# Kernel tuning notes

Hardware: AMD Instinct MI355X
Metric: run time of the kernel (lower is better)

The kernel has to match this reference:

```python
import jax, jax.numpy as jnp
import numpy as np

B, T, NPTS_PER, C, XDIM, YDIM, HEADS = 2, 4, 32768, 128, 200, 200, 4


def setup_inputs() -> dict:
    key = jax.random.key(0)
    ks = jax.random.split(key, 6)
    npts = B * T * NPTS_PER
    features = jax.random.normal(ks[0], (npts, C), dtype=jnp.float32)
    # chunk j of size NPTS_PER holds points of combined (batch*T + time) index j
    col0 = jnp.repeat(jnp.arange(B * T, dtype=jnp.int32), NPTS_PER)
    colx = jax.random.randint(ks[1], (npts,), 0, XDIM, dtype=jnp.int32)
    coly = jax.random.randint(ks[2], (npts,), 0, YDIM, dtype=jnp.int32)
    indices = jnp.stack([col0, colx, coly], axis=1)  # (Npts, 3)
    temp_embed = jax.random.normal(ks[3], (T, C), dtype=jnp.float32) * 0.02
    w_qkv = jax.random.normal(ks[4], (C, 3 * C), dtype=jnp.float32) / np.sqrt(C).astype(np.float32)
    w_out = jax.random.normal(ks[5], (C, C), dtype=jnp.float32) / np.sqrt(C).astype(np.float32)
    return {"features": features, "indices": indices, "temp_embed": temp_embed,
            "w_qkv": w_qkv, "w_out": w_out, "b": B, "t": T}


def reference(features, indices, temp_embed, w_qkv, w_out, b, t):
    npts, c = features.shape
    n = npts // (b * t)
    hd = c // HEADS
    scale = 1.0 / float(np.sqrt(hd))

    # temporal embedding: features + temp_embed[indices[:,0] % t]
    time_idx = indices[:, 0] % t
    f = features + temp_embed[time_idx]

    # chunk(b*t) + stack + rearrange 'N (b t) c -> (b N) t c'
    f = f.reshape(b, t, n, c).transpose(0, 2, 1, 3).reshape(b * n, t, c)

    # layer: multi-head self-attention over the temporal axis, take position t-1
    qkv = f @ w_qkv  # (bN, t, 3c)
    q, k, v = jnp.split(qkv, 3, axis=-1)
    split = lambda x: x.reshape(b * n, t, HEADS, hd).transpose(0, 2, 1, 3)  # (bN, H, t, hd)
    q, k, v = split(q), split(k), split(v)
    attn = jax.nn.softmax(jnp.einsum('bhqd,bhkd->bhqk', q, k) * scale, axis=-1)
    o = jnp.einsum('bhqk,bhkd->bhqd', attn, v)
    o = o.transpose(0, 2, 1, 3).reshape(b * n, t, c) @ w_out
    feat_out = o[:, t - 1]  # (bN, c)

    # indices: indices[:,0] //= t ; same window rearrange ; keep slice t-1
    idx = indices.at[:, 0].set(indices[:, 0] // t)
    idx_out = idx.reshape(b, t, n, 3).transpose(0, 2, 1, 3).reshape(b * n, t, 3)[:, t - 1]
    return feat_out, idx_out
```

## Files before the change

### kernel.cpp

```cpp
#include <hip/hip_runtime.h>

#define NPER   32768
#define TT     4
#define CDIM   128
#define NSEQ   65536
#define FEAT_OUT_ELEMS (NSEQ * CDIM)

constexpr int TSEQ = 16;
constexpr int ROWS = TSEQ * TT;
constexpr int KV_STRIDE = 257;
constexpr int Q_STRIDE  = 129;
constexpr int O_STRIDE  = 132;

typedef __attribute__((ext_vector_type(8))) short  short8;
typedef __attribute__((ext_vector_type(4))) float  f32x4;

__device__ __forceinline__ unsigned short f2bf(float x) {
    unsigned u = __float_as_uint(x);
    u = (u + 0x7FFFu + ((u >> 16) & 1u)) >> 16;
    return (unsigned short)u;
}
__device__ __forceinline__ float bf2f(unsigned short h) {
    return __uint_as_float(((unsigned)h) << 16);
}


__global__ void tqkv_kernel(const float* __restrict__ temp_embed,
                            const float* __restrict__ w_qkv,
                            float* __restrict__ tqkv) {
    int tid = blockIdx.x * blockDim.x + threadIdx.x;
    if (tid >= TT * 384) return;
    int t = tid / 384, col = tid - t * 384;
    float acc = 0.f;
#pragma unroll 8
    for (int k = 0; k < CDIM; ++k)
        acc = fmaf(temp_embed[t * CDIM + k], w_qkv[k * 384 + col], acc);
    tqkv[t * 384 + col] = acc;
}

__global__ void prep_weights(const float* __restrict__ w_qkv,
                             const float* __restrict__ w_out,
                             unsigned short* __restrict__ wkT_hi,
                             unsigned short* __restrict__ wkT_lo,
                             unsigned short* __restrict__ woT_hi,
                             unsigned short* __restrict__ woT_lo) {
    int id = blockIdx.x * 256 + threadIdx.x;
    if (id < 384 * 128) {
        int col = id >> 7, k = id & 127;
        float x = w_qkv[k * 384 + col];
        unsigned short h = f2bf(x);
        wkT_hi[id] = h;
        wkT_lo[id] = f2bf(x - bf2f(h));
    } else {
        int j = id - 384 * 128;
        int col = j >> 7, k = j & 127;
        float x = w_out[k * CDIM + col];
        unsigned short h = f2bf(x);
        woT_hi[j] = h;
        woT_lo[j] = f2bf(x - bf2f(h));
    }
}

__global__ __launch_bounds__(512, 2) void fused_mfma(
    const float* __restrict__ feat,
    const int*   __restrict__ indices,
    const float* __restrict__ tqkv,
    const unsigned short* __restrict__ wkT_hi,
    const unsigned short* __restrict__ wkT_lo,
    const unsigned short* __restrict__ woT_hi,
    const unsigned short* __restrict__ woT_lo,
    float* __restrict__ out) {

    __shared__ unsigned short AsH[ROWS * CDIM];
    __shared__ unsigned short AsL[ROWS * CDIM];
    __shared__ float KVs[ROWS * KV_STRIDE];
    __shared__ float Qs[TSEQ * Q_STRIDE];
    __shared__ float Os[TSEQ * O_STRIDE];
    __shared__ int   tix[ROWS];

    const int tid  = threadIdx.x;
    const int seq0 = blockIdx.x * TSEQ;

#pragma unroll
    for (int i = 0; i < 4; ++i) {
        int idx = tid + i * 512;
        int row = idx >> 5, c4 = idx & 31;
        int s = seq0 + (row >> 2), t = row & 3;
        int b = s >> 15, n = s & (NPER - 1);
        size_t p = (size_t)(b * TT + t) * NPER + n;
        float4 v = *reinterpret_cast<const float4*>(feat + p * CDIM + c4 * 4);
        unsigned short h0 = f2bf(v.x), h1 = f2bf(v.y), h2 = f2bf(v.z), h3 = f2bf(v.w);
        unsigned short l0 = f2bf(v.x - bf2f(h0)), l1 = f2bf(v.y - bf2f(h1));
        unsigned short l2 = f2bf(v.z - bf2f(h2)), l3 = f2bf(v.w - bf2f(h3));
        unsigned off = (unsigned)(row * 256 + c4 * 8) ^ ((unsigned)(row & 7) << 4);
        uint2 hp; hp.x = (unsigned)h0 | ((unsigned)h1 << 16); hp.y = (unsigned)h2 | ((unsigned)h3 << 16);
        uint2 lp; lp.x = (unsigned)l0 | ((unsigned)l1 << 16); lp.y = (unsigned)l2 | ((unsigned)l3 << 16);
        *reinterpret_cast<uint2*>(reinterpret_cast<char*>(AsH) + off) = hp;
        *reinterpret_cast<uint2*>(reinterpret_cast<char*>(AsL) + off) = lp;
        if (c4 == 0) tix[row] = indices[p * 3] & (TT - 1);
    }
    __syncthreads();

    const int w  = tid >> 6, l = tid & 63;
    const int lr = l & 15,  lh = l >> 4;

    f32x4 accKV[4][2];
#pragma unroll
    for (int mt = 0; mt < 4; ++mt)
#pragma unroll
        for (int j = 0; j < 2; ++j) accKV[mt][j] = (f32x4){0.f, 0.f, 0.f, 0.f};

#pragma unroll
    for (int kt = 0; kt < 4; ++kt) {
        const int kb = kt * 32 + lh * 8;
        const int c0 = (128 + (2 * w) * 16 + lr) * 128 + kb;
        const int c1 = c0 + 16 * 128;
        short8 B0h = *reinterpret_cast<const short8*>(wkT_hi + c0);
        short8 B0l = *reinterpret_cast<const short8*>(wkT_lo + c0);
        short8 B1h = *reinterpret_cast<const short8*>(wkT_hi + c1);
        short8 B1l = *reinterpret_cast<const short8*>(wkT_lo + c1);
#pragma unroll
        for (int mt = 0; mt < 4; ++mt) {
            int row = mt * 16 + lr;
            unsigned off = (unsigned)(row * 256 + kt * 64 + lh * 16) ^ ((unsigned)(row & 7) << 4);
            short8 Ah = *reinterpret_cast<const short8*>(reinterpret_cast<const char*>(AsH) + off);
            short8 Al = *reinterpret_cast<const short8*>(reinterpret_cast<const char*>(AsL) + off);
            accKV[mt][0] = __builtin_amdgcn_mfma_f32_16x16x32_bf16(Ah, B0h, accKV[mt][0], 0, 0, 0);
            accKV[mt][0] = __builtin_amdgcn_mfma_f32_16x16x32_bf16(Al, B0h, accKV[mt][0], 0, 0, 0);
            accKV[mt][0] = __builtin_amdgcn_mfma_f32_16x16x32_bf16(Ah, B0l, accKV[mt][0], 0, 0, 0);
            accKV[mt][1] = __builtin_amdgcn_mfma_f32_16x16x32_bf16(Ah, B1h, accKV[mt][1], 0, 0, 0);
            accKV[mt][1] = __builtin_amdgcn_mfma_f32_16x16x32_bf16(Al, B1h, accKV[mt][1], 0, 0, 0);
            accKV[mt][1] = __builtin_amdgcn_mfma_f32_16x16x32_bf16(Ah, B1l, accKV[mt][1], 0, 0, 0);
        }
    }
#pragma unroll
    for (int mt = 0; mt < 4; ++mt)
#pragma unroll
        for (int j = 0; j < 2; ++j) {
            int col = (2 * w + j) * 16 + lr;
#pragma unroll
            for (int r = 0; r < 4; ++r) {
                int row = mt * 16 + lh * 4 + r;
                int te  = tix[row];
                KVs[row * KV_STRIDE + col] = accKV[mt][j][r] + tqkv[te * 384 + 128 + col];
            }
        }

    f32x4 accQ = (f32x4){0.f, 0.f, 0.f, 0.f};
#pragma unroll
    for (int kt = 0; kt < 4; ++kt) {
        const int kb = kt * 32 + lh * 8;
        const int cq = (w * 16 + lr) * 128 + kb;
        short8 Bh = *reinterpret_cast<const short8*>(wkT_hi + cq);
        short8 Bl = *reinterpret_cast<const short8*>(wkT_lo + cq);
        int row = 4 * lr + 3;
        unsigned off = (unsigned)(row * 256 + kt * 64 + lh * 16) ^ ((unsigned)(row & 7) << 4);
        short8 Ah = *reinterpret_cast<const short8*>(reinterpret_cast<const char*>(AsH) + off);
        short8 Al = *reinterpret_cast<const short8*>(reinterpret_cast<const char*>(AsL) + off);
        accQ = __builtin_amdgcn_mfma_f32_16x16x32_bf16(Ah, Bh, accQ, 0, 0, 0);
        accQ = __builtin_amdgcn_mfma_f32_16x16x32_bf16(Al, Bh, accQ, 0, 0, 0);
        accQ = __builtin_amdgcn_mfma_f32_16x16x32_bf16(Ah, Bl, accQ, 0, 0, 0);
    }
#pragma unroll
    for (int r = 0; r < 4; ++r) {
        int s = lh * 4 + r, col = w * 16 + lr;
        int te = tix[4 * s + 3];
        Qs[s * Q_STRIDE + col] = accQ[r] + tqkv[te * 384 + col];
    }
    __syncthreads();

    {
        const float scale = 0.17677669529663687f;
        int pr = tid >> 3, j = tid & 7;
        int ls = pr >> 2, h = pr & 3;
        int d0 = h * 32 + j * 4;
        const float* qp = &Qs[ls * Q_STRIDE + d0];
        float q0 = qp[0], q1 = qp[1], q2 = qp[2], q3 = qp[3];
        float sc[4];
#pragma unroll
        for (int t2 = 0; t2 < 4; ++t2) {
            const float* kr = &KVs[(ls * 4 + t2) * KV_STRIDE + d0];
            float sum = fmaf(q0, kr[0], fmaf(q1, kr[1], fmaf(q2, kr[2], q3 * kr[3])));
            sum += __shfl_xor(sum, 1);
            sum += __shfl_xor(sum, 2);
            sum += __shfl_xor(sum, 4);
            sc[t2] = sum * scale;
        }
        float m = fmaxf(fmaxf(sc[0], sc[1]), fmaxf(sc[2], sc[3]));
        float p[4]; float Z = 0.f;
#pragma unroll
        for (int t2 = 0; t2 < 4; ++t2) { p[t2] = expf(sc[t2] - m); Z += p[t2]; }
        float rZ = 1.f / Z;
#pragma unroll
        for (int t2 = 0; t2 < 4; ++t2) p[t2] *= rZ;
#pragma unroll
        for (int d = 0; d < 4; ++d) {
            float o = 0.f;
#pragma unroll
            for (int t2 = 0; t2 < 4; ++t2)
                o = fmaf(p[t2], KVs[(ls * 4 + t2) * KV_STRIDE + 128 + d0 + d], o);
            Os[ls * O_STRIDE + d0 + d] = o;
        }
    }
    __syncthreads();

    f32x4 accO = (f32x4){0.f, 0.f, 0.f, 0.f};
#pragma unroll
    for (int kt = 0; kt < 4; ++kt) {
        const int kb = kt * 32 + lh * 8;
        const int co = (w * 16 + lr) * 128 + kb;
        short8 Bh = *reinterpret_cast<const short8*>(woT_hi + co);
        short8 Bl = *reinterpret_cast<const short8*>(woT_lo + co);
        const float* ap = &Os[lr * O_STRIDE + kb];
        float4 a01 = *reinterpret_cast<const float4*>(ap);
        float4 a23 = *reinterpret_cast<const float4*>(ap + 4);
        short8 Ah, Al;
        float av[8] = {a01.x, a01.y, a01.z, a01.w, a23.x, a23.y, a23.z, a23.w};
#pragma unroll
        for (int i = 0; i < 8; ++i) {
            unsigned short h = f2bf(av[i]);
            Ah[i] = (short)h;
            Al[i] = (short)f2bf(av[i] - bf2f(h));
        }
        accO = __builtin_amdgcn_mfma_f32_16x16x32_bf16(Ah, Bh, accO, 0, 0, 0);
        accO = __builtin_amdgcn_mfma_f32_16x16x32_bf16(Al, Bh, accO, 0, 0, 0);
        accO = __builtin_amdgcn_mfma_f32_16x16x32_bf16(Ah, Bl, accO, 0, 0, 0);
    }
#pragma unroll
    for (int r = 0; r < 4; ++r) {
        int s = lh * 4 + r, col = w * 16 + lr;
        out[(size_t)(seq0 + s) * CDIM + col] = accO[r];
    }

    if (tid < TSEQ * 3) {
        int ls = tid / 3, comp = tid - ls * 3;
        int sG = seq0 + ls;
        int b = sG >> 15, n = sG & (NPER - 1);
        int p3 = (b * TT + 3) * NPER + n;
        int val = (comp == 0) ? (indices[p3 * 3] >> 2)
                              : indices[p3 * 3 + comp];
        out[FEAT_OUT_ELEMS + (size_t)sG * 3 + comp] = (float)val;
    }
}

extern "C" void kernel_launch(void* const* d_in, const int* in_sizes, int n_in,
                              void* d_out, int out_size, void* d_ws, size_t ws_size,
                              hipStream_t stream) {
    const float* feat       = (const float*)d_in[0];
    const int*   indices    = (const int*)d_in[1];
    const float* temp_embed = (const float*)d_in[2];
    const float* w_qkv      = (const float*)d_in[3];
    const float* w_out      = (const float*)d_in[4];
    float* outp = (float*)d_out;

    char* ws = (char*)d_ws;
    float*          tqkv   = (float*)(ws);
    unsigned short* wkT_hi = (unsigned short*)(ws + 6144);
    unsigned short* wkT_lo = (unsigned short*)(ws + 104448);
    unsigned short* woT_hi = (unsigned short*)(ws + 202752);
    unsigned short* woT_lo = (unsigned short*)(ws + 235520);

    hipLaunchKernelGGL(tqkv_kernel, dim3(6), dim3(256), 0, stream,
                       temp_embed, w_qkv, tqkv);
    hipLaunchKernelGGL(prep_weights, dim3(256), dim3(256), 0, stream,
                       w_qkv, w_out, wkT_hi, wkT_lo, woT_hi, woT_lo);
    hipLaunchKernelGGL(fused_mfma, dim3(NSEQ / TSEQ), dim3(512), 0, stream,
                       feat, indices, tqkv, wkT_hi, wkT_lo, woT_hi, woT_lo, outp);
}
```

Measured before the change: 417.9 us.

## Double block to 1024 threads, split KV work per wave, pre-split attention output

The fused kernel now launches 1024-thread blocks (16 waves), so each wave computes a single 16-column KV tile instead of two. Only the first 8 waves do the Q and output projections. Attention uses 16 lanes per head with float2 loads, and its output is written to LDS already split into bf16 hi/lo, so the output GEMM no longer converts it. Strides are padded for aligned vector access. The intent is more parallelism and fewer registers per thread, at the cost of idle waves during the Q and output phases and fewer blocks resident per CU.

```diff
diff --git a/kernel.cpp b/kernel.cpp
--- a/kernel.cpp
+++ b/kernel.cpp
@@ -8,9 +8,9 @@
 
 constexpr int TSEQ = 16;
 constexpr int ROWS = TSEQ * TT;
-constexpr int KV_STRIDE = 257;
-constexpr int Q_STRIDE  = 129;
-constexpr int O_STRIDE  = 132;
+constexpr int KV_W = 260;
+constexpr int Q_W  = 132;
+constexpr int O_W  = 136;
 
 typedef __attribute__((ext_vector_type(8))) short  short8;
 typedef __attribute__((ext_vector_type(4))) float  f32x4;
@@ -61,7 +61,7 @@
     }
 }
 
-__global__ __launch_bounds__(512, 2) void fused_mfma(
+__global__ __launch_bounds__(1024, 1) void fused_mfma(
     const float* __restrict__ feat,
     const int*   __restrict__ indices,
     const float* __restrict__ tqkv,
@@ -73,17 +73,18 @@
 
     __shared__ unsigned short AsH[ROWS * CDIM];
     __shared__ unsigned short AsL[ROWS * CDIM];
-    __shared__ float KVs[ROWS * KV_STRIDE];
-    __shared__ float Qs[TSEQ * Q_STRIDE];
-    __shared__ float Os[TSEQ * O_STRIDE];
-    __shared__ int   tix[ROWS];
+    __shared__ float KVs[ROWS * KV_W];
+    __shared__ float Qs[TSEQ * Q_W];
+    __shared__ unsigned short OsH[TSEQ * O_W];
+    __shared__ unsigned short OsL[TSEQ * O_W];
+    __shared__ int tix[ROWS];
 
     const int tid  = threadIdx.x;
     const int seq0 = blockIdx.x * TSEQ;
 
 #pragma unroll
-    for (int i = 0; i < 4; ++i) {
-        int idx = tid + i * 512;
+    for (int i = 0; i < 2; ++i) {
+        int idx = tid + i * 1024;
         int row = idx >> 5, c4 = idx & 31;
         int s = seq0 + (row >> 2), t = row & 3;
         int b = s >> 15, n = s & (NPER - 1);
@@ -104,86 +105,80 @@
     const int w  = tid >> 6, l = tid & 63;
     const int lr = l & 15,  lh = l >> 4;
 
-    f32x4 accKV[4][2];
-#pragma unroll
-    for (int mt = 0; mt < 4; ++mt)
-#pragma unroll
-        for (int j = 0; j < 2; ++j) accKV[mt][j] = (f32x4){0.f, 0.f, 0.f, 0.f};
-
+    f32x4 acc[4];
+#pragma unroll
+    for (int mt = 0; mt < 4; ++mt) acc[mt] = (f32x4){0.f, 0.f, 0.f, 0.f};
 #pragma unroll
     for (int kt = 0; kt < 4; ++kt) {
         const int kb = kt * 32 + lh * 8;
-        const int c0 = (128 + (2 * w) * 16 + lr) * 128 + kb;
-        const int c1 = c0 + 16 * 128;
-        short8 B0h = *reinterpret_cast<const short8*>(wkT_hi + c0);
-        short8 B0l = *reinterpret_cast<const short8*>(wkT_lo + c0);
-        short8 B1h = *reinterpret_cast<const short8*>(wkT_hi + c1);
-        short8 B1l = *reinterpret_cast<const short8*>(wkT_lo + c1);
+        const int c0 = (128 + w * 16 + lr) * 128 + kb;
+        short8 Bh = *reinterpret_cast<const short8*>(wkT_hi + c0);
+        short8 Bl = *reinterpret_cast<const short8*>(wkT_lo + c0);
 #pragma unroll
         for (int mt = 0; mt < 4; ++mt) {
             int row = mt * 16 + lr;
             unsigned off = (unsigned)(row * 256 + kt * 64 + lh * 16) ^ ((unsigned)(row & 7) << 4);
             short8 Ah = *reinterpret_cast<const short8*>(reinterpret_cast<const char*>(AsH) + off);
             short8 Al = *reinterpret_cast<const short8*>(reinterpret_cast<const char*>(AsL) + off);
-            accKV[mt][0] = __builtin_amdgcn_mfma_f32_16x16x32_bf16(Ah, B0h, accKV[mt][0], 0, 0, 0);
-            accKV[mt][0] = __builtin_amdgcn_mfma_f32_16x16x32_bf16(Al, B0h, accKV[mt][0], 0, 0, 0);
-            accKV[mt][0] = __builtin_amdgcn_mfma_f32_16x16x32_bf16(Ah, B0l, accKV[mt][0], 0, 0, 0);
-            accKV[mt][1] = __builtin_amdgcn_mfma_f32_16x16x32_bf16(Ah, B1h, accKV[mt][1], 0, 0, 0);
-            accKV[mt][1] = __builtin_amdgcn_mfma_f32_16x16x32_bf16(Al, B1h, accKV[mt][1], 0, 0, 0);
-            accKV[mt][1] = __builtin_amdgcn_mfma_f32_16x16x32_bf16(Ah, B1l, accKV[mt][1], 0, 0, 0);
-        }
-    }
-#pragma unroll
-    for (int mt = 0; mt < 4; ++mt)
-#pragma unroll
-        for (int j = 0; j < 2; ++j) {
-            int col = (2 * w + j) * 16 + lr;
-#pragma unroll
-            for (int r = 0; r < 4; ++r) {
-                int row = mt * 16 + lh * 4 + r;
-                int te  = tix[row];
-                KVs[row * KV_STRIDE + col] = accKV[mt][j][r] + tqkv[te * 384 + 128 + col];
-            }
-        }
+            acc[mt] = __builtin_amdgcn_mfma_f32_16x16x32_bf16(Ah, Bh, acc[mt], 0, 0, 0);
+            acc[mt] = __builtin_amdgcn_mfma_f32_16x16x32_bf16(Al, Bh, acc[mt], 0, 0, 0);
+            acc[mt] = __builtin_amdgcn_mfma_f32_16x16x32_bf16(Ah, Bl, acc[mt], 0, 0, 0);
+        }
+    }
 
     f32x4 accQ = (f32x4){0.f, 0.f, 0.f, 0.f};
-#pragma unroll
-    for (int kt = 0; kt < 4; ++kt) {
-        const int kb = kt * 32 + lh * 8;
-        const int cq = (w * 16 + lr) * 128 + kb;
-        short8 Bh = *reinterpret_cast<const short8*>(wkT_hi + cq);
-        short8 Bl = *reinterpret_cast<const short8*>(wkT_lo + cq);
-        int row = 4 * lr + 3;
-        unsigned off = (unsigned)(row * 256 + kt * 64 + lh * 16) ^ ((unsigned)(row & 7) << 4);
-        short8 Ah = *reinterpret_cast<const short8*>(reinterpret_cast<const char*>(AsH) + off);
-        short8 Al = *reinterpret_cast<const short8*>(reinterpret_cast<const char*>(AsL) + off);
-        accQ = __builtin_amdgcn_mfma_f32_16x16x32_bf16(Ah, Bh, accQ, 0, 0, 0);
-        accQ = __builtin_amdgcn_mfma_f32_16x16x32_bf16(Al, Bh, accQ, 0, 0, 0);
-        accQ = __builtin_amdgcn_mfma_f32_16x16x32_bf16(Ah, Bl, accQ, 0, 0, 0);
-    }
-#pragma unroll
-    for (int r = 0; r < 4; ++r) {
-        int s = lh * 4 + r, col = w * 16 + lr;
-        int te = tix[4 * s + 3];
-        Qs[s * Q_STRIDE + col] = accQ[r] + tqkv[te * 384 + col];
+    if (w < 8) {
+#pragma unroll
+        for (int kt = 0; kt < 4; ++kt) {
+            const int kb = kt * 32 + lh * 8;
+            const int cq = (w * 16 + lr) * 128 + kb;
+            short8 Bh = *reinterpret_cast<const short8*>(wkT_hi + cq);
+            short8 Bl = *reinterpret_cast<const short8*>(wkT_lo + cq);
+            int row = 4 * lr + 3;
+            unsigned off = (unsigned)(row * 256 + kt * 64 + lh * 16) ^ ((unsigned)(row & 7) << 4);
+            short8 Ah = *reinterpret_cast<const short8*>(reinterpret_cast<const char*>(AsH) + off);
+            short8 Al = *reinterpret_cast<const short8*>(reinterpret_cast<const char*>(AsL) + off);
+            accQ = __builtin_amdgcn_mfma_f32_16x16x32_bf16(Ah, Bh, accQ, 0, 0, 0);
+            accQ = __builtin_amdgcn_mfma_f32_16x16x32_bf16(Al, Bh, accQ, 0, 0, 0);
+            accQ = __builtin_amdgcn_mfma_f32_16x16x32_bf16(Ah, Bl, accQ, 0, 0, 0);
+        }
+    }
+
+#pragma unroll
+    for (int mt = 0; mt < 4; ++mt) {
+        int col = w * 16 + lr;
+#pragma unroll
+        for (int r = 0; r < 4; ++r) {
+            int row = mt * 16 + lh * 4 + r;
+            int te  = tix[row];
+            KVs[row * KV_W + col] = acc[mt][r] + tqkv[te * 384 + 128 + col];
+        }
+    }
+    if (w < 8) {
+#pragma unroll
+        for (int r = 0; r < 4; ++r) {
+            int s = lh * 4 + r, col = w * 16 + lr;
+            int te = tix[4 * s + 3];
+            Qs[s * Q_W + col] = accQ[r] + tqkv[te * 384 + col];
+        }
     }
     __syncthreads();
 
     {
         const float scale = 0.17677669529663687f;
-        int pr = tid >> 3, j = tid & 7;
+        int pr = tid >> 4, j = tid & 15;
         int ls = pr >> 2, h = pr & 3;
-        int d0 = h * 32 + j * 4;
-        const float* qp = &Qs[ls * Q_STRIDE + d0];
-        float q0 = qp[0], q1 = qp[1], q2 = qp[2], q3 = qp[3];
+        int d0 = h * 32 + j * 2;
+        float2 qv = *reinterpret_cast<const float2*>(&Qs[ls * Q_W + d0]);
         float sc[4];
 #pragma unroll
         for (int t2 = 0; t2 < 4; ++t2) {
-            const float* kr = &KVs[(ls * 4 + t2) * KV_STRIDE + d0];
-            float sum = fmaf(q0, kr[0], fmaf(q1, kr[1], fmaf(q2, kr[2], q3 * kr[3])));
+            float2 kv = *reinterpret_cast<const float2*>(&KVs[(ls * 4 + t2) * KV_W + d0]);
+            float sum = fmaf(qv.x, kv.x, qv.y * kv.y);
             sum += __shfl_xor(sum, 1);
             sum += __shfl_xor(sum, 2);
             sum += __shfl_xor(sum, 4);
+            sum += __shfl_xor(sum, 8);
             sc[t2] = sum * scale;
         }
         float m = fmaxf(fmaxf(sc[0], sc[1]), fmaxf(sc[2], sc[3]));
@@ -191,45 +186,40 @@
 #pragma unroll
         for (int t2 = 0; t2 < 4; ++t2) { p[t2] = expf(sc[t2] - m); Z += p[t2]; }
         float rZ = 1.f / Z;
-#pragma unroll
-        for (int t2 = 0; t2 < 4; ++t2) p[t2] *= rZ;
-#pragma unroll
-        for (int d = 0; d < 4; ++d) {
-            float o = 0.f;
-#pragma unroll
-            for (int t2 = 0; t2 < 4; ++t2)
-                o = fmaf(p[t2], KVs[(ls * 4 + t2) * KV_STRIDE + 128 + d0 + d], o);
-            Os[ls * O_STRIDE + d0 + d] = o;
-        }
+        float o0 = 0.f, o1 = 0.f;
+#pragma unroll
+        for (int t2 = 0; t2 < 4; ++t2) {
+            float2 vv = *reinterpret_cast<const float2*>(&KVs[(ls * 4 + t2) * KV_W + 128 + d0]);
+            float pp = p[t2] * rZ;
+            o0 = fmaf(pp, vv.x, o0);
+            o1 = fmaf(pp, vv.y, o1);
+        }
+        unsigned short h0 = f2bf(o0), h1 = f2bf(o1);
+        unsigned short g0 = f2bf(o0 - bf2f(h0)), g1 = f2bf(o1 - bf2f(h1));
+        *reinterpret_cast<unsigned*>(&OsH[ls * O_W + d0]) = (unsigned)h0 | ((unsigned)h1 << 16);
+        *reinterpret_cast<unsigned*>(&OsL[ls * O_W + d0]) = (unsigned)g0 | ((unsigned)g1 << 16);
     }
     __syncthreads();
 
-    f32x4 accO = (f32x4){0.f, 0.f, 0.f, 0.f};
-#pragma unroll
-    for (int kt = 0; kt < 4; ++kt) {
-        const int kb = kt * 32 + lh * 8;
-        const int co = (w * 16 + lr) * 128 + kb;
-        short8 Bh = *reinterpret_cast<const short8*>(woT_hi + co);
-        short8 Bl = *reinterpret_cast<const short8*>(woT_lo + co);
-        const float* ap = &Os[lr * O_STRIDE + kb];
-        float4 a01 = *reinterpret_cast<const float4*>(ap);
-        float4 a23 = *reinterpret_cast<const float4*>(ap + 4);
-        short8 Ah, Al;
-        float av[8] = {a01.x, a01.y, a01.z, a01.w, a23.x, a23.y, a23.z, a23.w};
-#pragma unroll
-        for (int i = 0; i < 8; ++i) {
-            unsigned short h = f2bf(av[i]);
-            Ah[i] = (short)h;
-            Al[i] = (short)f2bf(av[i] - bf2f(h));
-        }
-        accO = __builtin_amdgcn_mfma_f32_16x16x32_bf16(Ah, Bh, accO, 0, 0, 0);
-        accO = __builtin_amdgcn_mfma_f32_16x16x32_bf16(Al, Bh, accO, 0, 0, 0);
-        accO = __builtin_amdgcn_mfma_f32_16x16x32_bf16(Ah, Bl, accO, 0, 0, 0);
-    }
-#pragma unroll
-    for (int r = 0; r < 4; ++r) {
-        int s = lh * 4 + r, col = w * 16 + lr;
-        out[(size_t)(seq0 + s) * CDIM + col] = accO[r];
+    if (w < 8) {
+        f32x4 accO = (f32x4){0.f, 0.f, 0.f, 0.f};
+#pragma unroll
+        for (int kt = 0; kt < 4; ++kt) {
+            const int kb = kt * 32 + lh * 8;
+            const int co = (w * 16 + lr) * 128 + kb;
+            short8 Bh = *reinterpret_cast<const short8*>(woT_hi + co);
+            short8 Bl = *reinterpret_cast<const short8*>(woT_lo + co);
+            short8 Ah = *reinterpret_cast<const short8*>(&OsH[lr * O_W + kb]);
+            short8 Al = *reinterpret_cast<const short8*>(&OsL[lr * O_W + kb]);
+            accO = __builtin_amdgcn_mfma_f32_16x16x32_bf16(Ah, Bh, accO, 0, 0, 0);
+            accO = __builtin_amdgcn_mfma_f32_16x16x32_bf16(Al, Bh, accO, 0, 0, 0);
+            accO = __builtin_amdgcn_mfma_f32_16x16x32_bf16(Ah, Bl, accO, 0, 0, 0);
+        }
+#pragma unroll
+        for (int r = 0; r < 4; ++r) {
+            int s = lh * 4 + r, col = w * 16 + lr;
+            out[(size_t)(seq0 + s) * CDIM + col] = accO[r];
+        }
     }
 
     if (tid < TSEQ * 3) {
@@ -264,6 +254,6 @@
                        temp_embed, w_qkv, tqkv);
     hipLaunchKernelGGL(prep_weights, dim3(256), dim3(256), 0, stream,
                        w_qkv, w_out, wkT_hi, wkT_lo, woT_hi, woT_lo);
-    hipLaunchKernelGGL(fused_mfma, dim3(NSEQ / TSEQ), dim3(512), 0, stream,
+    hipLaunchKernelGGL(fused_mfma, dim3(NSEQ / TSEQ), dim3(1024), 0, stream,
                        feat, indices, tqkv, wkT_hi, wkT_lo, woT_hi, woT_lo, outp);
 }
```

New measurement: 383.9 us. -8.1%, faster.
